# Performance work log

Hardware: AMD Instinct MI355X
Metric: run time of the kernel (lower is better)

## Reference

```python
import jax, jax.numpy as jnp
import numpy as np

N = 10000
E = 160000
D_IN, D_H = 512, 256


def _glorot(key, shape):
    fan_in, fan_out = shape[0], shape[1]
    lim = jnp.sqrt(6.0 / (fan_in + fan_out)).astype(jnp.float32)
    return jax.random.uniform(key, shape, jnp.float32, -lim, lim)


def setup_inputs() -> dict:
    key = jax.random.key(0)
    ks = jax.random.split(key, 12)
    x = jax.random.normal(ks[0], (N, D_IN), jnp.float32)
    edge_index = jax.random.randint(ks[1], (2, E), 0, N, jnp.int64)
    return {
        "x": x,
        "edge_index": edge_index,
        # SAGEConv: lin_l acts on aggregated neighbors (with bias), lin_r on root
        "W_l": _glorot(ks[2], (D_IN, D_H)),
        "b_l": jnp.zeros((D_H,), jnp.float32),
        "W_r": _glorot(ks[3], (D_IN, D_H)),
        "Wa": _glorot(ks[4], (256, 128)), "ba": jnp.zeros((128,), jnp.float32),
        "W1": _glorot(ks[5], (128, 64)),  "b1": jnp.zeros((64,), jnp.float32),
        "W2": _glorot(ks[6], (64, 32)),   "b2": jnp.zeros((32,), jnp.float32),
        "W3": _glorot(ks[7], (32, 3)),    "b3": jnp.zeros((3,), jnp.float32),
    }


def _sage_mean_aggr(x, edge_index):
    # PyG convention: message x_j = x[src], aggregated (mean) at dst
    src, dst = edge_index[0], edge_index[1]
    sums = jax.ops.segment_sum(x[src], dst, num_segments=N)          # [N, D_IN]
    cnt = jax.ops.segment_sum(jnp.ones((E,), x.dtype), dst, num_segments=N)
    return sums / jnp.maximum(cnt, 1.0)[:, None]


def _pairwise_l2(x):
    # cdist(x, x, p=2) via norm trick; zero-clamp for numerical safety
    sq = jnp.sum(x * x, axis=-1)                                      # [N]
    d2 = sq[:, None] + sq[None, :] - 2.0 * (x @ x.T)                  # [N, N]
    d2 = jnp.maximum(d2, 0.0)
    safe = jnp.where(d2 > 0, d2, 1.0)
    return jnp.where(d2 > 0, jnp.sqrt(safe), 0.0)


def reference(x, edge_index, W_l, b_l, W_r, Wa, ba, W1, b1, W2, b2, W3, b3):
    aggr = _sage_mean_aggr(x, edge_index)
    h = aggr @ W_l + b_l + x @ W_r                                    # SAGEConv out [N, 256]
    h = jax.nn.relu(h)
    h = jax.nn.relu(h @ Wa + ba)
    h = jax.nn.relu(h @ W1 + b1)
    h = jax.nn.relu(h @ W2 + b2)
    h = h @ W3 + b3                                                   # [N, 3]
    return _pairwise_l2(h)                                            # [N, N]
```

## Files before the change

### kernel.cpp

```cpp
#include <hip/hip_runtime.h>

#define N_NODES 10000
#define N_EDGES 160000

__global__ void count_kernel(const int* __restrict__ ei, int* __restrict__ deg) {
    int e = blockIdx.x * blockDim.x + threadIdx.x;
    if (e < N_EDGES) {
        int dst = ei[N_EDGES + e];
        atomicAdd(&deg[dst], 1);
    }
}

__global__ void scanA_kernel(const int* __restrict__ deg, int* __restrict__ row_start,
                             int* __restrict__ chunk_tot) {
    __shared__ int s[256];
    int c = blockIdx.x, tid = threadIdx.x;
    int i = c * 256 + tid;
    int v = (i < N_NODES) ? deg[i] : 0;
    s[tid] = v;
    __syncthreads();
    for (int off = 1; off < 256; off <<= 1) {
        int t = (tid >= off) ? s[tid - off] : 0;
        __syncthreads();
        s[tid] += t;
        __syncthreads();
    }
    if (i < N_NODES) row_start[i + 1] = s[tid];
    if (tid == 255) chunk_tot[c] = s[255];
}

__global__ void scanC_kernel(int* __restrict__ row_start, const int* __restrict__ chunk_tot) {
    int c = blockIdx.x, tid = threadIdx.x;
    int off = 0;
    for (int cc = 0; cc < c; ++cc) off += chunk_tot[cc];
    int i = c * 256 + tid;
    if (i < N_NODES) row_start[i + 1] += off;
    if (c == 0 && tid == 0) row_start[0] = 0;
}

__global__ void scatter_kernel(const int* __restrict__ ei, const int* __restrict__ row_start,
                               int* __restrict__ cursor, int* __restrict__ csr_src) {
    int e = blockIdx.x * blockDim.x + threadIdx.x;
    if (e < N_EDGES) {
        int src = ei[e];
        int dst = ei[N_EDGES + e];
        int p = atomicAdd(&cursor[dst], 1);
        csr_src[row_start[dst] + p] = src;
    }
}

__global__ __launch_bounds__(256) void zgemm_kernel(const float* __restrict__ x,
                                                    const float* __restrict__ W_l,
                                                    const float* __restrict__ W_r,
                                                    float* __restrict__ Z) {
    const int BK = 32;
    __shared__ float As[32][68];
    __shared__ float Bs[32][68];
    int tid = threadIdx.x;
    int rowbase = blockIdx.y * 64;
    int colbase = blockIdx.x * 64;
    const float* B = (colbase < 256) ? W_l : W_r;
    int bcol = colbase & 255;
    float acc[4][4] = {};

    for (int kt = 0; kt < 512; kt += BK) {
        {
            int r = tid >> 3;
            int c4 = (tid & 7) * 4;
#pragma unroll
            for (int h = 0; h < 2; ++h) {
                int row = rowbase + r + h * 32;
                int arow = min(row, N_NODES - 1);
                float4 v = *(const float4*)(x + (size_t)arow * 512 + kt + c4);
                As[c4 + 0][r + h * 32] = v.x;
                As[c4 + 1][r + h * 32] = v.y;
                As[c4 + 2][r + h * 32] = v.z;
                As[c4 + 3][r + h * 32] = v.w;
            }
        }
        {
            int kr = tid >> 4;
            int c4 = (tid & 15) * 4;
#pragma unroll
            for (int h = 0; h < 2; ++h) {
                int k = kt + kr + h * 16;
                float4 v = *(const float4*)(B + (size_t)k * 256 + bcol + c4);
                *(float4*)&Bs[kr + h * 16][c4] = v;
            }
        }
        __syncthreads();
        int tm = (tid & 15) * 4;
        int tn = (tid >> 4) * 4;
#pragma unroll
        for (int kk = 0; kk < BK; ++kk) {
            float4 av = *(const float4*)&As[kk][tm];
            float4 bv = *(const float4*)&Bs[kk][tn];
            float a[4] = {av.x, av.y, av.z, av.w};
            float b[4] = {bv.x, bv.y, bv.z, bv.w};
#pragma unroll
            for (int i = 0; i < 4; ++i)
#pragma unroll
                for (int j = 0; j < 4; ++j) acc[i][j] += a[i] * b[j];
        }
        __syncthreads();
    }

    int tm = (tid & 15) * 4;
    int tn = (tid >> 4) * 4;
#pragma unroll
    for (int i = 0; i < 4; ++i) {
        int row = rowbase + tm + i;
        if (row >= N_NODES) continue;
        float* zr = Z + (size_t)row * 512 + colbase + tn;
        *(float4*)(zr) = make_float4(acc[i][0], acc[i][1], acc[i][2], acc[i][3]);
    }
}

__global__ __launch_bounds__(256) void aggr_fused_kernel(const float* __restrict__ z,
                                                         const int* __restrict__ csr_src,
                                                         const int* __restrict__ row_start,
                                                         const float* __restrict__ b_l,
                                                         float* __restrict__ h1) {
    int lane = threadIdx.x & 63;
    int dst = blockIdx.x * 4 + (threadIdx.x >> 6);
    int beg = row_start[dst], end = row_start[dst + 1];
    float4 acc = make_float4(0.f, 0.f, 0.f, 0.f);
    int i = beg;
    for (; i + 1 < end; i += 2) {
        int s0 = csr_src[i];
        int s1 = csr_src[i + 1];
        float4 v0 = *((const float4*)(z + (size_t)s0 * 512) + lane);
        float4 v1 = *((const float4*)(z + (size_t)s1 * 512) + lane);
        acc.x += v0.x + v1.x; acc.y += v0.y + v1.y;
        acc.z += v0.z + v1.z; acc.w += v0.w + v1.w;
    }
    if (i < end) {
        int s0 = csr_src[i];
        float4 v0 = *((const float4*)(z + (size_t)s0 * 512) + lane);
        acc.x += v0.x; acc.y += v0.y; acc.z += v0.z; acc.w += v0.w;
    }
    float inv = 1.0f / (float)max(end - beg, 1);
    float4 r = *((const float4*)(z + (size_t)dst * 512 + 256) + lane);
    float4 bb = *((const float4*)b_l + lane);
    float4 o;
    o.x = fmaxf(fmaf(acc.x, inv, r.x + bb.x), 0.f);
    o.y = fmaxf(fmaf(acc.y, inv, r.y + bb.y), 0.f);
    o.z = fmaxf(fmaf(acc.z, inv, r.z + bb.z), 0.f);
    o.w = fmaxf(fmaf(acc.w, inv, r.w + bb.w), 0.f);
    *((float4*)(h1 + (size_t)dst * 256) + lane) = o;
}

template <bool RELU>
__global__ __launch_bounds__(256) void gemm_kernel(const float* __restrict__ A,
                                                   const float* __restrict__ B,
                                                   const float* __restrict__ bias,
                                                   float* __restrict__ C,
                                                   int M, int K, int N) {
    const int BK = 32;
    __shared__ float As[32][68];
    __shared__ float Bs[32][68];
    int tid = threadIdx.x;
    int rowbase = blockIdx.y * 64;
    int colbase = blockIdx.x * 64;
    float acc[4][4] = {};

    for (int kt = 0; kt < K; kt += BK) {
        {
            int r = tid >> 3;
            int c4 = (tid & 7) * 4;
#pragma unroll
            for (int h = 0; h < 2; ++h) {
                int row = rowbase + r + h * 32;
                int arow = min(row, M - 1);
                float4 v = *(const float4*)(A + (size_t)arow * K + kt + c4);
                As[c4 + 0][r + h * 32] = v.x;
                As[c4 + 1][r + h * 32] = v.y;
                As[c4 + 2][r + h * 32] = v.z;
                As[c4 + 3][r + h * 32] = v.w;
            }
        }
        {
            int kr = tid >> 4;
            int c4 = (tid & 15) * 4;
#pragma unroll
            for (int h = 0; h < 2; ++h) {
                int k = kt + kr + h * 16;
                int col = colbase + c4;
                float4 v;
                if (col + 4 <= N) {
                    v = *(const float4*)(B + (size_t)k * N + col);
                } else {
                    v.x = (col + 0 < N) ? B[(size_t)k * N + col + 0] : 0.f;
                    v.y = (col + 1 < N) ? B[(size_t)k * N + col + 1] : 0.f;
                    v.z = (col + 2 < N) ? B[(size_t)k * N + col + 2] : 0.f;
                    v.w = (col + 3 < N) ? B[(size_t)k * N + col + 3] : 0.f;
                }
                *(float4*)&Bs[kr + h * 16][c4] = v;
            }
        }
        __syncthreads();
        int tm = (tid & 15) * 4;
        int tn = (tid >> 4) * 4;
#pragma unroll
        for (int kk = 0; kk < BK; ++kk) {
            float4 av = *(const float4*)&As[kk][tm];
            float4 bv = *(const float4*)&Bs[kk][tn];
            float a[4] = {av.x, av.y, av.z, av.w};
            float b[4] = {bv.x, bv.y, bv.z, bv.w};
#pragma unroll
            for (int i = 0; i < 4; ++i)
#pragma unroll
                for (int j = 0; j < 4; ++j) acc[i][j] += a[i] * b[j];
        }
        __syncthreads();
    }

    int tm = (tid & 15) * 4;
    int tn = (tid >> 4) * 4;
#pragma unroll
    for (int i = 0; i < 4; ++i) {
        int row = rowbase + tm + i;
        if (row >= M) continue;
#pragma unroll
        for (int j = 0; j < 4; ++j) {
            int col = colbase + tn + j;
            if (col >= N) continue;
            float v = acc[i][j] + bias[col];
            if (RELU) v = fmaxf(v, 0.f);
            C[(size_t)row * N + col] = v;
        }
    }
}

__global__ __launch_bounds__(256) void dist_kernel(const float* __restrict__ y,
                                                   float* __restrict__ out) {
    __shared__ float sa[192];
    __shared__ float sb[192];
    int rb = blockIdx.y * 64;
    int cb = blockIdx.x * 64;
    int tid = threadIdx.x;
    if (tid < 192) {
        int ga = rb * 3 + tid;
        sa[tid] = (ga < 3 * N_NODES) ? y[ga] : 0.f;
        int gb = cb * 3 + tid;
        sb[tid] = (gb < 3 * N_NODES) ? y[gb] : 0.f;
    }
    __syncthreads();
    int ty = tid >> 4;
    int tx = tid & 15;
    int c0 = tx * 4;
#pragma unroll
    for (int i = 0; i < 4; ++i) {
        int r = ty * 4 + i;
        int row = rb + r;
        if (row >= N_NODES) continue;
        float ax = sa[r * 3 + 0], ay = sa[r * 3 + 1], az = sa[r * 3 + 2];
        float res[4];
#pragma unroll
        for (int j = 0; j < 4; ++j) {
            int cc = c0 + j;
            float dx = ax - sb[cc * 3 + 0];
            float dy = ay - sb[cc * 3 + 1];
            float dz = az - sb[cc * 3 + 2];
            res[j] = sqrtf(dx * dx + dy * dy + dz * dz);
        }
        int col = cb + c0;
        size_t base = (size_t)row * N_NODES + col;
        if (col + 4 <= N_NODES) {
            *(float4*)(out + base) = make_float4(res[0], res[1], res[2], res[3]);
        } else {
#pragma unroll
            for (int j = 0; j < 4; ++j)
                if (col + j < N_NODES) out[base + j] = res[j];
        }
    }
}

extern "C" void kernel_launch(void* const* d_in, const int* in_sizes, int n_in,
                              void* d_out, int out_size, void* d_ws, size_t ws_size,
                              hipStream_t stream) {
    const float* x   = (const float*)d_in[0];
    const int*   ei  = (const int*)d_in[1];
    const float* W_l = (const float*)d_in[2];
    const float* b_l = (const float*)d_in[3];
    const float* W_r = (const float*)d_in[4];
    const float* Wa  = (const float*)d_in[5];
    const float* ba  = (const float*)d_in[6];
    const float* W1  = (const float*)d_in[7];
    const float* b1  = (const float*)d_in[8];
    const float* W2  = (const float*)d_in[9];
    const float* b2  = (const float*)d_in[10];
    const float* W3  = (const float*)d_in[11];
    const float* b3  = (const float*)d_in[12];

    float* out = (float*)d_out;
    float* z    = out;
    float* h1   = out + 5120000;
    float* h2   = out + 7680000;
    float* h3   = out + 8960000;
    float* h4   = out + 9600000;

    float* y        = (float*)d_ws;
    int* deg        = (int*)d_ws + 30000;
    int* row_start  = (int*)d_ws + 40000;
    int* cursor     = (int*)d_ws + 50016;
    int* chunk_tot  = (int*)d_ws + 60016;
    int* csr_src    = (int*)d_ws + 60064;

    hipMemsetAsync(deg, 0, N_NODES * sizeof(int), stream);
    hipMemsetAsync(cursor, 0, N_NODES * sizeof(int), stream);

    zgemm_kernel<<<dim3(8, 157), 256, 0, stream>>>(x, W_l, W_r, z);

    count_kernel<<<(N_EDGES + 255) / 256, 256, 0, stream>>>(ei, deg);
    scanA_kernel<<<40, 256, 0, stream>>>(deg, row_start, chunk_tot);
    scanC_kernel<<<40, 256, 0, stream>>>(row_start, chunk_tot);
    scatter_kernel<<<(N_EDGES + 255) / 256, 256, 0, stream>>>(ei, row_start, cursor, csr_src);

    aggr_fused_kernel<<<2500, 256, 0, stream>>>(z, csr_src, row_start, b_l, h1);

    dim3 b256(256);
    gemm_kernel<true><<<dim3(2, 157), b256, 0, stream>>>(h1, Wa, ba, h2, N_NODES, 256, 128);
    gemm_kernel<true><<<dim3(1, 157), b256, 0, stream>>>(h2, W1, b1, h3, N_NODES, 128, 64);
    gemm_kernel<true><<<dim3(1, 157), b256, 0, stream>>>(h3, W2, b2, h4, N_NODES, 64, 32);
    gemm_kernel<false><<<dim3(1, 157), b256, 0, stream>>>(h4, W3, b3, y, N_NODES, 32, 3);

    dist_kernel<<<dim3(157, 157), b256, 0, stream>>>(y, out);
}
```

Measured before the change: 647.9 us.

## Fuse MLP tail layers into one kernel and enlarge zgemm row tile

The four small per-layer GEMM launches are replaced by a single tail kernel. Each block takes 64 rows of h1 and runs all the MLP layers on them, keeping the intermediate activations transposed in shared memory, so h2, h3 and h4 no longer round-trip through global memory and three launches disappear. The zgemm tile also grows from 64 to 128 rows per block (8x4 outputs per thread) to reuse more data per load. In exchange, the tail kernel runs only 157 blocks with heavy shared memory use, which limits occupancy, and the larger zgemm tile raises register pressure.

```diff
diff --git a/kernel.cpp b/kernel.cpp
--- a/kernel.cpp
+++ b/kernel.cpp
@@ -54,21 +54,24 @@
                                                     const float* __restrict__ W_r,
                                                     float* __restrict__ Z) {
     const int BK = 32;
-    __shared__ float As[32][68];
+    __shared__ float As[32][132];
     __shared__ float Bs[32][68];
     int tid = threadIdx.x;
-    int rowbase = blockIdx.y * 64;
+    int rowbase = blockIdx.y * 128;
     int colbase = blockIdx.x * 64;
     const float* B = (colbase < 256) ? W_l : W_r;
     int bcol = colbase & 255;
-    float acc[4][4] = {};
+    float acc[8][4] = {};
+
+    int tm = (tid >> 4) * 8;
+    int tn = (tid & 15) * 4;
 
     for (int kt = 0; kt < 512; kt += BK) {
         {
             int r = tid >> 3;
             int c4 = (tid & 7) * 4;
 #pragma unroll
-            for (int h = 0; h < 2; ++h) {
+            for (int h = 0; h < 4; ++h) {
                 int row = rowbase + r + h * 32;
                 int arow = min(row, N_NODES - 1);
                 float4 v = *(const float4*)(x + (size_t)arow * 512 + kt + c4);
@@ -89,26 +92,23 @@
             }
         }
         __syncthreads();
-        int tm = (tid & 15) * 4;
-        int tn = (tid >> 4) * 4;
 #pragma unroll
         for (int kk = 0; kk < BK; ++kk) {
-            float4 av = *(const float4*)&As[kk][tm];
+            float4 av0 = *(const float4*)&As[kk][tm];
+            float4 av1 = *(const float4*)&As[kk][tm + 4];
             float4 bv = *(const float4*)&Bs[kk][tn];
-            float a[4] = {av.x, av.y, av.z, av.w};
+            float a[8] = {av0.x, av0.y, av0.z, av0.w, av1.x, av1.y, av1.z, av1.w};
             float b[4] = {bv.x, bv.y, bv.z, bv.w};
 #pragma unroll
-            for (int i = 0; i < 4; ++i)
+            for (int i = 0; i < 8; ++i)
 #pragma unroll
                 for (int j = 0; j < 4; ++j) acc[i][j] += a[i] * b[j];
         }
         __syncthreads();
     }
 
-    int tm = (tid & 15) * 4;
-    int tn = (tid >> 4) * 4;
-#pragma unroll
-    for (int i = 0; i < 4; ++i) {
+#pragma unroll
+    for (int i = 0; i < 8; ++i) {
         int row = rowbase + tm + i;
         if (row >= N_NODES) continue;
         float* zr = Z + (size_t)row * 512 + colbase + tn;
@@ -150,84 +150,152 @@
     *((float4*)(h1 + (size_t)dst * 256) + lane) = o;
 }
 
-template <bool RELU>
-__global__ __launch_bounds__(256) void gemm_kernel(const float* __restrict__ A,
-                                                   const float* __restrict__ B,
-                                                   const float* __restrict__ bias,
-                                                   float* __restrict__ C,
-                                                   int M, int K, int N) {
-    const int BK = 32;
+__global__ __launch_bounds__(256) void tail_kernel(const float* __restrict__ h1,
+                                                   const float* __restrict__ Wa, const float* __restrict__ ba,
+                                                   const float* __restrict__ W1, const float* __restrict__ b1,
+                                                   const float* __restrict__ W2, const float* __restrict__ b2,
+                                                   const float* __restrict__ W3, const float* __restrict__ b3,
+                                                   float* __restrict__ y) {
     __shared__ float As[32][68];
-    __shared__ float Bs[32][68];
+    __shared__ float SB[32][132];
+    __shared__ float H2T[128][68];
+    __shared__ float H3T[64][68];
+    __shared__ float H4T[32][68];
     int tid = threadIdx.x;
-    int rowbase = blockIdx.y * 64;
-    int colbase = blockIdx.x * 64;
-    float acc[4][4] = {};
-
-    for (int kt = 0; kt < K; kt += BK) {
+    int rowbase = blockIdx.x * 64;
+
+    int tm = (tid & 15) * 4;
+
+    {
+        int tn = (tid >> 4) * 8;
+        float acc[4][8] = {};
+        for (int kt = 0; kt < 256; kt += 32) {
+            {
+                int r = tid >> 3;
+                int c4 = (tid & 7) * 4;
+#pragma unroll
+                for (int h = 0; h < 2; ++h) {
+                    int row = rowbase + r + h * 32;
+                    int arow = min(row, N_NODES - 1);
+                    float4 v = *(const float4*)(h1 + (size_t)arow * 256 + kt + c4);
+                    As[c4 + 0][r + h * 32] = v.x;
+                    As[c4 + 1][r + h * 32] = v.y;
+                    As[c4 + 2][r + h * 32] = v.z;
+                    As[c4 + 3][r + h * 32] = v.w;
+                }
+            }
+            {
+                int kr = tid >> 3;
+                int cc = (tid & 7) * 16;
+                const float* bp = Wa + (size_t)(kt + kr) * 128 + cc;
+                *(float4*)&SB[kr][cc + 0]  = *(const float4*)(bp + 0);
+                *(float4*)&SB[kr][cc + 4]  = *(const float4*)(bp + 4);
+                *(float4*)&SB[kr][cc + 8]  = *(const float4*)(bp + 8);
+                *(float4*)&SB[kr][cc + 12] = *(const float4*)(bp + 12);
+            }
+            __syncthreads();
+#pragma unroll
+            for (int kk = 0; kk < 32; ++kk) {
+                float4 av = *(const float4*)&As[kk][tm];
+                float4 bv0 = *(const float4*)&SB[kk][tn];
+                float4 bv1 = *(const float4*)&SB[kk][tn + 4];
+                float a[4] = {av.x, av.y, av.z, av.w};
+                float b[8] = {bv0.x, bv0.y, bv0.z, bv0.w, bv1.x, bv1.y, bv1.z, bv1.w};
+#pragma unroll
+                for (int i = 0; i < 4; ++i)
+#pragma unroll
+                    for (int j = 0; j < 8; ++j) acc[i][j] += a[i] * b[j];
+            }
+            __syncthreads();
+        }
+#pragma unroll
+        for (int j = 0; j < 8; ++j) {
+            float bj = ba[tn + j];
+#pragma unroll
+            for (int i = 0; i < 4; ++i)
+                H2T[tn + j][tm + i] = fmaxf(acc[i][j] + bj, 0.f);
+        }
+        __syncthreads();
+    }
+
+    {
+        int tn = (tid >> 4) * 4;
+        float acc[4][4] = {};
+        for (int kt = 0; kt < 128; kt += 32) {
+            {
+                int kr = tid >> 3;
+                int cc = (tid & 7) * 8;
+                const float* bp = W1 + (size_t)(kt + kr) * 64 + cc;
+                *(float4*)&SB[kr][cc + 0] = *(const float4*)(bp + 0);
+                *(float4*)&SB[kr][cc + 4] = *(const float4*)(bp + 4);
+            }
+            __syncthreads();
+#pragma unroll
+            for (int kk = 0; kk < 32; ++kk) {
+                float4 av = *(const float4*)&H2T[kt + kk][tm];
+                float4 bv = *(const float4*)&SB[kk][tn];
+                float a[4] = {av.x, av.y, av.z, av.w};
+                float b[4] = {bv.x, bv.y, bv.z, bv.w};
+#pragma unroll
+                for (int i = 0; i < 4; ++i)
+#pragma unroll
+                    for (int j = 0; j < 4; ++j) acc[i][j] += a[i] * b[j];
+            }
+            __syncthreads();
+        }
+#pragma unroll
+        for (int j = 0; j < 4; ++j) {
+            float bj = b1[tn + j];
+#pragma unroll
+            for (int i = 0; i < 4; ++i)
+                H3T[tn + j][tm + i] = fmaxf(acc[i][j] + bj, 0.f);
+        }
+    }
+
+    {
+        float* SBf = &SB[0][0];
         {
-            int r = tid >> 3;
-            int c4 = (tid & 7) * 4;
-#pragma unroll
-            for (int h = 0; h < 2; ++h) {
-                int row = rowbase + r + h * 32;
-                int arow = min(row, M - 1);
-                float4 v = *(const float4*)(A + (size_t)arow * K + kt + c4);
-                As[c4 + 0][r + h * 32] = v.x;
-                As[c4 + 1][r + h * 32] = v.y;
-                As[c4 + 2][r + h * 32] = v.z;
-                As[c4 + 3][r + h * 32] = v.w;
-            }
-        }
-        {
-            int kr = tid >> 4;
-            int c4 = (tid & 15) * 4;
-#pragma unroll
-            for (int h = 0; h < 2; ++h) {
-                int k = kt + kr + h * 16;
-                int col = colbase + c4;
-                float4 v;
-                if (col + 4 <= N) {
-                    v = *(const float4*)(B + (size_t)k * N + col);
-                } else {
-                    v.x = (col + 0 < N) ? B[(size_t)k * N + col + 0] : 0.f;
-                    v.y = (col + 1 < N) ? B[(size_t)k * N + col + 1] : 0.f;
-                    v.z = (col + 2 < N) ? B[(size_t)k * N + col + 2] : 0.f;
-                    v.w = (col + 3 < N) ? B[(size_t)k * N + col + 3] : 0.f;
-                }
-                *(float4*)&Bs[kr + h * 16][c4] = v;
-            }
-        }
-        __syncthreads();
-        int tm = (tid & 15) * 4;
-        int tn = (tid >> 4) * 4;
-#pragma unroll
-        for (int kk = 0; kk < BK; ++kk) {
-            float4 av = *(const float4*)&As[kk][tm];
-            float4 bv = *(const float4*)&Bs[kk][tn];
+            int r = tid >> 2;
+            int c = (tid & 3) * 8;
+            const float* bp = W2 + (size_t)r * 32 + c;
+            *(float4*)&SBf[r * 36 + c + 0] = *(const float4*)(bp + 0);
+            *(float4*)&SBf[r * 36 + c + 4] = *(const float4*)(bp + 4);
+        }
+        __syncthreads();
+        int tn = (tid >> 4) * 2;
+        float acc[4][2] = {};
+#pragma unroll
+        for (int kk = 0; kk < 64; ++kk) {
+            float4 av = *(const float4*)&H3T[kk][tm];
+            float b0 = SBf[kk * 36 + tn + 0];
+            float b1v = SBf[kk * 36 + tn + 1];
             float a[4] = {av.x, av.y, av.z, av.w};
-            float b[4] = {bv.x, bv.y, bv.z, bv.w};
+#pragma unroll
+            for (int i = 0; i < 4; ++i) {
+                acc[i][0] += a[i] * b0;
+                acc[i][1] += a[i] * b1v;
+            }
+        }
+#pragma unroll
+        for (int j = 0; j < 2; ++j) {
+            float bj = b2[tn + j];
 #pragma unroll
             for (int i = 0; i < 4; ++i)
-#pragma unroll
-                for (int j = 0; j < 4; ++j) acc[i][j] += a[i] * b[j];
-        }
-        __syncthreads();
-    }
-
-    int tm = (tid & 15) * 4;
-    int tn = (tid >> 4) * 4;
-#pragma unroll
-    for (int i = 0; i < 4; ++i) {
-        int row = rowbase + tm + i;
-        if (row >= M) continue;
-#pragma unroll
-        for (int j = 0; j < 4; ++j) {
-            int col = colbase + tn + j;
-            if (col >= N) continue;
-            float v = acc[i][j] + bias[col];
-            if (RELU) v = fmaxf(v, 0.f);
-            C[(size_t)row * N + col] = v;
+                H4T[tn + j][tm + i] = fmaxf(acc[i][j] + bj, 0.f);
+        }
+        __syncthreads();
+    }
+
+    {
+        int row = tid >> 2;
+        int col = tid & 3;
+        if (col < 3) {
+            float s = b3[col];
+#pragma unroll
+            for (int k = 0; k < 32; ++k)
+                s += H4T[k][row] * W3[k * 3 + col];
+            int grow = rowbase + row;
+            if (grow < N_NODES) y[(size_t)grow * 3 + col] = s;
         }
     }
 }
@@ -296,9 +364,6 @@
     float* out = (float*)d_out;
     float* z    = out;
     float* h1   = out + 5120000;
-    float* h2   = out + 7680000;
-    float* h3   = out + 8960000;
-    float* h4   = out + 9600000;
 
     float* y        = (float*)d_ws;
     int* deg        = (int*)d_ws + 30000;
@@ -310,7 +375,7 @@
     hipMemsetAsync(deg, 0, N_NODES * sizeof(int), stream);
     hipMemsetAsync(cursor, 0, N_NODES * sizeof(int), stream);
 
-    zgemm_kernel<<<dim3(8, 157), 256, 0, stream>>>(x, W_l, W_r, z);
+    zgemm_kernel<<<dim3(8, 79), 256, 0, stream>>>(x, W_l, W_r, z);
 
     count_kernel<<<(N_EDGES + 255) / 256, 256, 0, stream>>>(ei, deg);
     scanA_kernel<<<40, 256, 0, stream>>>(deg, row_start, chunk_tot);
@@ -319,11 +384,7 @@
 
     aggr_fused_kernel<<<2500, 256, 0, stream>>>(z, csr_src, row_start, b_l, h1);
 
-    dim3 b256(256);
-    gemm_kernel<true><<<dim3(2, 157), b256, 0, stream>>>(h1, Wa, ba, h2, N_NODES, 256, 128);
-    gemm_kernel<true><<<dim3(1, 157), b256, 0, stream>>>(h2, W1, b1, h3, N_NODES, 128, 64);
-    gemm_kernel<true><<<dim3(1, 157), b256, 0, stream>>>(h3, W2, b2, h4, N_NODES, 64, 32);
-    gemm_kernel<false><<<dim3(1, 157), b256, 0, stream>>>(h4, W3, b3, y, N_NODES, 32, 3);
-
-    dist_kernel<<<dim3(157, 157), b256, 0, stream>>>(y, out);
-}
+    tail_kernel<<<157, 256, 0, stream>>>(h1, Wa, ba, W1, b1, W2, b2, W3, b3, y);
+
+    dist_kernel<<<dim3(157, 157), 256, 0, stream>>>(y, out);
+}
```

Measured after the change: 634.1 us. 1.02x faster.
